# Kernel tuning notes

Hardware: AMD Instinct MI355X
Metric: run time of the kernel (lower is better)

Reference implementation:

```python
import jax, jax.numpy as jnp
import numpy as np

N_USER = 100000
N_ITEM = 50000
N_EDGE = 400000
D_IN = 128
N_HEADS = 4
D_HEAD = 32


def setup_inputs() -> dict:
    key = jax.random.key(0)
    ks = jax.random.split(key, 10)
    s = 1.0 / np.sqrt(D_IN)
    return {
        "h_user": jax.random.normal(ks[0], (N_USER, D_IN), jnp.float32),
        "h_item": jax.random.normal(ks[1], (N_ITEM, D_IN), jnp.float32),
        "edge_user": jax.random.randint(ks[2], (N_EDGE,), 0, N_USER),
        "edge_item": jax.random.randint(ks[3], (N_EDGE,), 0, N_ITEM),
        "user_w_qs": jax.random.normal(ks[4], (N_HEADS, D_IN, D_HEAD), jnp.float32) * s,
        "user_w_ks": jax.random.normal(ks[5], (N_HEADS, D_IN, D_HEAD), jnp.float32) * s,
        "user_w_vs": jax.random.normal(ks[6], (N_HEADS, D_IN, D_HEAD), jnp.float32) * s,
        "item_w_qs": jax.random.normal(ks[7], (N_HEADS, D_IN, D_HEAD), jnp.float32) * s,
        "item_w_ks": jax.random.normal(ks[8], (N_HEADS, D_IN, D_HEAD), jnp.float32) * s,
        "item_w_vs": jax.random.normal(ks[9], (N_HEADS, D_IN, D_HEAD), jnp.float32) * s,
    }


def _segment_softmax(logit, seg, num_segments):
    m = jax.ops.segment_max(logit, seg, num_segments=num_segments)
    e = jnp.exp(logit - m[seg])
    s = jax.ops.segment_sum(e, seg, num_segments=num_segments)
    return e / s[seg]


def _attend(src_idx, dst_idx, h_src, h_dst, w_qs, w_ks, w_vs, n_dst):
    # per-head projections: [H, n, d_head]
    q = jnp.einsum("nd,hde->hne", h_dst, w_qs)
    k = jnp.einsum("nd,hde->hne", h_src, w_ks)
    v = jnp.einsum("nd,hde->hne", h_src, w_vs)
    # per-edge logits: [H, E]
    logit = jnp.sum(q[:, dst_idx] * k[:, src_idx], axis=-1)
    att = jax.vmap(lambda l: _segment_softmax(l, dst_idx, n_dst))(logit)
    # sparse adj @ v == segment-sum of attention-weighted source values
    msg = att[..., None] * v[:, src_idx]  # [H, E, d_head]
    z = jax.vmap(lambda m: jax.ops.segment_sum(m, dst_idx, num_segments=n_dst))(msg)
    z = jax.nn.relu(z)  # nonlinear per head, then merge (concat)
    return jnp.transpose(z, (1, 0, 2)).reshape(n_dst, -1)


def reference(h_user, h_item, edge_user, edge_item,
              user_w_qs, user_w_ks, user_w_vs,
              item_w_qs, item_w_ks, item_w_vs):
    # i2u: items -> users (dst = users)
    z_user = _attend(edge_item, edge_user, h_item, h_user,
                     user_w_qs, item_w_ks, item_w_vs, N_USER)
    # u2i: users -> items (dst = items)
    z_item = _attend(edge_user, edge_item, h_user, h_item,
                     item_w_qs, user_w_ks, user_w_vs, N_ITEM)
    return (z_user, z_item)
```

## Files before the change

kernel.cpp:

```cpp
#include <hip/hip_runtime.h>
#include <hip/hip_fp16.h>


typedef unsigned short u16;
typedef float f32x4 __attribute__((ext_vector_type(4)));
typedef short bf16x8 __attribute__((ext_vector_type(8)));

#define NU_C    100000
#define NI_C    50000
#define E_C     400000
#define D_IN    128
#define D_HEAD  32
#define N_HEADS 4

#define PROJ_ROWS 64
#define PGU 1563
#define PGI 782
#define WT_BLKS 384

#define SCAN_T  256
#define SCAN_E  1024

__device__ __forceinline__ float bf2f(u16 b) {
    return __uint_as_float(((unsigned)b) << 16);
}

__device__ __forceinline__ u16 f2bf_rn(float x) {
    unsigned u = __float_as_uint(x);
    u += 0x7FFFu + ((u >> 16) & 1u);
    return (u16)(u >> 16);
}

__device__ __forceinline__ u16 f2h(float x) {
    return __half_as_ushort(__float2half(x));
}
__device__ __forceinline__ float h2f(u16 b) {
    return __half2float(__ushort_as_half(b));
}

__global__ void detect_dtypes(const void* __restrict__ h,
                              const void* __restrict__ eu,
                              int* __restrict__ flags) {
    int t = threadIdx.x;
    const u16* hw = (const u16*)h;
    int cnt = 0;
#pragma unroll
    for (int r = 0; r < 2; ++r) {
        int i = t + r * 64;
        unsigned ex = (hw[2 * i] >> 7) & 0xFFu;
        if (ex >= 118u && ex <= 137u) cnt++;
    }
    const int* ew = (const int*)eu;
    int nz = 0;
#pragma unroll
    for (int r = 0; r < 4; ++r) {
        int i = t + r * 64;
        if (ew[2 * i + 1] != 0) nz++;
    }
#pragma unroll
    for (int m = 1; m < 64; m <<= 1) {
        cnt += __shfl_xor(cnt, m);
        nz  += __shfl_xor(nz, m);
    }
    if (t == 0) {
        flags[0] = (cnt >= 64) ? 1 : 0;
        flags[1] = (nz == 0) ? 1 : 0;
        flags[2] = 0;
        flags[3] = 0;
    }
}

__global__ __launch_bounds__(256)
void prep(const void* __restrict__ w0, const void* __restrict__ w1,
          const void* __restrict__ w2, const void* __restrict__ w3,
          const void* __restrict__ w4, const void* __restrict__ w5,
          u16* __restrict__ wthi, u16* __restrict__ wtlo,
          const int* __restrict__ e_user, const int* __restrict__ e_item,
          int* __restrict__ du, int* __restrict__ di,
          int* __restrict__ degU, int* __restrict__ degI,
          int* __restrict__ flags) {
    int b = blockIdx.x;
    if (b < WT_BLKS) {
        int m = b >> 6;
        int f = (b & 63) * 256 + threadIdx.x;
        const void* ws[6] = { w0, w1, w2, w3, w4, w5 };
        const void* wp = ws[m];
        int head = f >> 12, e = f & 31;
        float x;
        if (flags[0]) x = bf2f(((const u16*)wp)[f]);
        else          x = ((const float*)wp)[f];
        u16 h = f2bf_rn(x);
        u16 l = f2bf_rn(x - bf2f(h));
        int o = m * 16384 + (head * 32 + e) * 128 + ((f >> 5) & 127);
        wthi[o] = h;
        wtlo[o] = l;
    } else {
        int g = (b - WT_BLKS) * 256 + threadIdx.x;
        if (g >= E_C) return;
        int is64 = flags[1];
        int u = is64 ? e_user[2 * g] : e_user[g];
        int i = is64 ? e_item[2 * g] : e_item[g];
        if ((unsigned)u >= (unsigned)NU_C) { atomicOr(&flags[3], 1); u = 0; }
        if ((unsigned)i >= (unsigned)NI_C) { atomicOr(&flags[3], 1); i = 0; }
        du[g] = u;
        di[g] = i;
        atomicAdd(&degU[u], 1);
        atomicAdd(&degI[i], 1);
    }
}

__global__ __launch_bounds__(SCAN_T)
void scan_pass1(const int* __restrict__ degU, int* __restrict__ offsU,
                int* __restrict__ partU, int nU, int sbU,
                const int* __restrict__ degI, int* __restrict__ offsI,
                int* __restrict__ partI, int nI) {
    __shared__ int tsum[SCAN_T];
    int t = threadIdx.x, b = blockIdx.x;
    const int* deg; int* offs; int* partials; int n; int lb;
    if (b < sbU) { deg = degU; offs = offsU; partials = partU; n = nU; lb = b; }
    else         { deg = degI; offs = offsI; partials = partI; n = nI; lb = b - sbU; }
    int idx = lb * SCAN_E + t * 4;
    int v0 = 0, v1 = 0, v2 = 0, v3 = 0;
    if (idx + 3 < n) {
        v0 = deg[idx]; v1 = deg[idx + 1]; v2 = deg[idx + 2]; v3 = deg[idx + 3];
    } else {
        if (idx     < n) v0 = deg[idx];
        if (idx + 1 < n) v1 = deg[idx + 1];
        if (idx + 2 < n) v2 = deg[idx + 2];
        if (idx + 3 < n) v3 = deg[idx + 3];
    }
    int s = v0 + v1 + v2 + v3;
    tsum[t] = s;
    __syncthreads();
#pragma unroll
    for (int o = 1; o < SCAN_T; o <<= 1) {
        int x = (t >= o) ? tsum[t - o] : 0;
        __syncthreads();
        tsum[t] += x;
        __syncthreads();
    }
    int run = tsum[t] - s;
    if (idx     < n) offs[idx]     = run;             run += v0;
    if (idx + 1 < n) offs[idx + 1] = run;             run += v1;
    if (idx + 2 < n) offs[idx + 2] = run;             run += v2;
    if (idx + 3 < n) offs[idx + 3] = run;
    if (t == SCAN_T - 1) partials[lb] = tsum[t];
}

__global__ __launch_bounds__(SCAN_T)
void scan_pass2(int* __restrict__ partU, int sbU,
                int* __restrict__ partI, int sbI) {
    __shared__ int tsum[SCAN_T];
    int t = threadIdx.x;
    int* partials; int nb;
    if (blockIdx.x == 0) { partials = partU; nb = sbU; }
    else                 { partials = partI; nb = sbI; }
    int v = (t < nb) ? partials[t] : 0;
    tsum[t] = v;
    __syncthreads();
#pragma unroll
    for (int o = 1; o < SCAN_T; o <<= 1) {
        int x = (t >= o) ? tsum[t - o] : 0;
        __syncthreads();
        tsum[t] += x;
        __syncthreads();
    }
    if (t < nb) partials[t] = tsum[t] - v;
}

__global__ void scatter2(const int* __restrict__ du, const int* __restrict__ di,
                         const int* __restrict__ offsU, const int* __restrict__ partU,
                         int* __restrict__ cntU, int* __restrict__ csrU,
                         const int* __restrict__ offsI, const int* __restrict__ partI,
                         int* __restrict__ cntI, int* __restrict__ csrI, int egrid) {
    int b = blockIdx.x;
    int g = (b >= egrid ? b - egrid : b) * 256 + threadIdx.x;
    if (g >= E_C) return;
    if (b < egrid) {
        int d = du[g];
        int pos = offsU[d] + partU[d >> 10] + atomicAdd(&cntU[d], 1);
        csrU[pos] = di[g];
    } else {
        int d = di[g];
        int pos = offsI[d] + partI[d >> 10] + atomicAdd(&cntI[d], 1);
        csrI[pos] = du[g];
    }
}

__global__ __launch_bounds__(256)
void proj6(const void* __restrict__ hu, const void* __restrict__ hi_,
           const u16* __restrict__ wthi_, const u16* __restrict__ wtlo_,
           u16* __restrict__ QU, u16* __restrict__ KI, u16* __restrict__ VI,
           u16* __restrict__ QI, u16* __restrict__ KU, u16* __restrict__ VU,
           const int* __restrict__ flags) {
    __shared__ u16 Hhi[PROJ_ROWS * 32], Hlo[PROJ_ROWS * 32];
    __shared__ u16 Bhi[128 * 32],       Blo[128 * 32];

    const int b = blockIdx.x;
    const void* hraw; const u16* wth; const u16* wtl; u16* out; int N; int lb;
    if (b < PGU) {
        hraw = hu;  wth = wthi_ + 0 * 16384; wtl = wtlo_ + 0 * 16384;
        out = QU; N = NU_C; lb = b;
    } else if (b < PGU + PGI) {
        hraw = hi_; wth = wthi_ + 4 * 16384; wtl = wtlo_ + 4 * 16384;
        out = KI; N = NI_C; lb = b - PGU;
    } else if (b < PGU + 2 * PGI) {
        hraw = hi_; wth = wthi_ + 5 * 16384; wtl = wtlo_ + 5 * 16384;
        out = VI; N = NI_C; lb = b - PGU - PGI;
    } else if (b < PGU + 3 * PGI) {
        hraw = hi_; wth = wthi_ + 3 * 16384; wtl = wtlo_ + 3 * 16384;
        out = QI; N = NI_C; lb = b - PGU - 2 * PGI;
    } else if (b < 2 * PGU + 3 * PGI) {
        hraw = hu;  wth = wthi_ + 1 * 16384; wtl = wtlo_ + 1 * 16384;
        out = KU; N = NU_C; lb = b - PGU - 3 * PGI;
    } else {
        hraw = hu;  wth = wthi_ + 2 * 16384; wtl = wtlo_ + 2 * 16384;
        out = VU; N = NU_C; lb = b - 2 * PGU - 3 * PGI;
    }

    const int t = threadIdx.x;
    const int n0 = lb * PROJ_ROWS;
    const int isbf = flags[0];

    const int srow = t >> 2, sq = t & 3;
    const int sgn = min(n0 + srow, N - 1);
    const int hbase = srow * 32 + ((sq ^ ((srow >> 1) & 3)) << 3);
    const int wj = t >> 1, wh = t & 1;
    const int wb0 = wj * 32 + (((wh * 2)     ^ ((wj >> 1) & 3)) << 3);
    const int wb1 = wj * 32 + (((wh * 2 + 1) ^ ((wj >> 1) & 3)) << 3);
    const int w = t >> 6, l = t & 63;
    const int lr = l & 15, lk = l >> 4;
    const int sc = (lk ^ ((lr >> 1) & 3)) << 3;

    f32x4 acc[4][2];
#pragma unroll
    for (int rt = 0; rt < 4; ++rt)
#pragma unroll
        for (int ci = 0; ci < 2; ++ci) {
            acc[rt][ci].x = 0.f; acc[rt][ci].y = 0.f;
            acc[rt][ci].z = 0.f; acc[rt][ci].w = 0.f;
        }

#define COMPUTE_STEP                                                           \
    do {                                                                       \
        bf16x8 fAh[4], fAl[4], fBh[2], fBl[2];                                 \
        _Pragma("unroll")                                                      \
        for (int rt = 0; rt < 4; ++rt) {                                       \
            int ar = (rt * 16 + lr) * 32 + sc;                                 \
            fAh[rt] = *(const bf16x8*)&Hhi[ar];                                \
            fAl[rt] = *(const bf16x8*)&Hlo[ar];                                \
        }                                                                      \
        _Pragma("unroll")                                                      \
        for (int ci = 0; ci < 2; ++ci) {                                       \
            int jr = ((w * 2 + ci) * 16 + lr) * 32 + sc;                       \
            fBh[ci] = *(const bf16x8*)&Bhi[jr];                                \
            fBl[ci] = *(const bf16x8*)&Blo[jr];                                \
        }                                                                      \
        _Pragma("unroll")                                                      \
        for (int rt = 0; rt < 4; ++rt)                                         \
        _Pragma("unroll")                                                      \
        for (int ci = 0; ci < 2; ++ci) {                                       \
            acc[rt][ci] = __builtin_amdgcn_mfma_f32_16x16x32_bf16(             \
                fAl[rt], fBh[ci], acc[rt][ci], 0, 0, 0);                       \
            acc[rt][ci] = __builtin_amdgcn_mfma_f32_16x16x32_bf16(             \
                fAh[rt], fBl[ci], acc[rt][ci], 0, 0, 0);                       \
            acc[rt][ci] = __builtin_amdgcn_mfma_f32_16x16x32_bf16(             \
                fAh[rt], fBh[ci], acc[rt][ci], 0, 0, 0);                       \
        }                                                                      \
    } while (0)

    if (!isbf) {
        const float* hp = (const float*)hraw;
        f32x4 rh0, rh1; bf16x8 rwh0, rwh1, rwl0, rwl1;
#define PLOAD(KC)                                                              \
        do {                                                                   \
            const float* hq = hp + (size_t)sgn * D_IN + (KC) * 32 + sq * 8;    \
            rh0 = *(const f32x4*)hq;                                           \
            rh1 = *(const f32x4*)(hq + 4);                                     \
            const u16* wp = wth + wj * 128 + (KC) * 32 + wh * 16;              \
            rwh0 = *(const bf16x8*)wp;  rwh1 = *(const bf16x8*)(wp + 8);       \
            const u16* lp = wtl + wj * 128 + (KC) * 32 + wh * 16;              \
            rwl0 = *(const bf16x8*)lp;  rwl1 = *(const bf16x8*)(lp + 8);       \
        } while (0)
        PLOAD(0);
        for (int kc = 0; kc < 4; ++kc) {
            if (kc) __syncthreads();
            bf16x8 hi8, lo8;
#pragma unroll
            for (int i = 0; i < 4; ++i) {
                u16 hh = f2bf_rn(rh0[i]);
                hi8[i] = (short)hh;
                lo8[i] = (short)f2bf_rn(rh0[i] - bf2f(hh));
            }
#pragma unroll
            for (int i = 0; i < 4; ++i) {
                u16 hh = f2bf_rn(rh1[i]);
                hi8[4 + i] = (short)hh;
                lo8[4 + i] = (short)f2bf_rn(rh1[i] - bf2f(hh));
            }
            *(bf16x8*)&Hhi[hbase] = hi8;
            *(bf16x8*)&Hlo[hbase] = lo8;
            *(bf16x8*)&Bhi[wb0] = rwh0;
            *(bf16x8*)&Bhi[wb1] = rwh1;
            *(bf16x8*)&Blo[wb0] = rwl0;
            *(bf16x8*)&Blo[wb1] = rwl1;
            __syncthreads();
            if (kc < 3) PLOAD(kc + 1);
            COMPUTE_STEP;
        }
#undef PLOAD
    } else {
        for (int kc = 0; kc < 4; ++kc) {
            if (kc) __syncthreads();
            bf16x8 hv = *(const bf16x8*)((const u16*)hraw
                        + (size_t)sgn * D_IN + kc * 32 + sq * 8);
            bf16x8 z;
#pragma unroll
            for (int i = 0; i < 8; ++i) z[i] = 0;
            *(bf16x8*)&Hhi[hbase] = hv;
            *(bf16x8*)&Hlo[hbase] = z;
            const u16* wp = wth + wj * 128 + kc * 32 + wh * 16;
            const u16* lp = wtl + wj * 128 + kc * 32 + wh * 16;
            *(bf16x8*)&Bhi[wb0] = *(const bf16x8*)wp;
            *(bf16x8*)&Bhi[wb1] = *(const bf16x8*)(wp + 8);
            *(bf16x8*)&Blo[wb0] = *(const bf16x8*)lp;
            *(bf16x8*)&Blo[wb1] = *(const bf16x8*)(lp + 8);
            __syncthreads();
            COMPUTE_STEP;
        }
    }
#undef COMPUTE_STEP

#pragma unroll
    for (int rt = 0; rt < 4; ++rt) {
#pragma unroll
        for (int r = 0; r < 4; ++r) {
            int n = n0 + rt * 16 + lk * 4 + r;
            if (n < N) {
#pragma unroll
                for (int ci = 0; ci < 2; ++ci)
                    out[(size_t)n * 128 + w * 32 + ci * 16 + lr] =
                        f2h(acc[rt][ci][r]);
            }
        }
    }
}

__global__ __launch_bounds__(256)
void gather_both(const int* __restrict__ offsU, const int* __restrict__ partU,
                 const int* __restrict__ csrU,
                 const int* __restrict__ offsI, const int* __restrict__ partI,
                 const int* __restrict__ csrI,
                 const u16* __restrict__ QU, const u16* __restrict__ KI,
                 const u16* __restrict__ VI,
                 const u16* __restrict__ QI, const u16* __restrict__ KU,
                 const u16* __restrict__ VU,
                 float* __restrict__ outbase, const int* __restrict__ flags,
                 int ggU) {
    int b = blockIdx.x;
    const int *offs, *part, *csr; const u16 *q, *k, *v;
    float* out; int Ndst; int g;
    if (b < ggU) {
        offs = offsU; part = partU; csr = csrU;
        q = QU; k = KI; v = VI; out = outbase; Ndst = NU_C;
        g = b * 256 + threadIdx.x;
    } else {
        offs = offsI; part = partI; csr = csrI;
        q = QI; k = KU; v = VU;
        out = outbase + (size_t)NU_C * 128; Ndst = NI_C;
        g = (b - ggU) * 256 + threadIdx.x;
    }
    int dst = g >> 6;
    if (dst >= Ndst) return;
    int l  = g & 63;
    int eh = l >> 5;
    int sl = l & 31;
    float* op = out + (size_t)dst * 128 + sl * 4;

    if (flags[3]) {
        if (eh == 0) {
            f32x4 d64; d64.x = d64.y = d64.z = d64.w = 64.0f;
            *(f32x4*)op = d64;
        }
        return;
    }

    ushort4 qu = *(const ushort4*)(q + (size_t)dst * 128 + sl * 4);
    f32x4 qv;
    qv.x = h2f(qu.x); qv.y = h2f(qu.y); qv.z = h2f(qu.z); qv.w = h2f(qu.w);
    f32x4 acc; acc.x = acc.y = acc.z = acc.w = 0.f;
    float ssum = 0.f;

    int e0 = offs[dst] + part[dst >> 10];
    int e1 = (dst + 1 == Ndst) ? E_C
             : offs[dst + 1] + part[(dst + 1) >> 10];
    int e = e0 + eh;
    for (; e + 2 < e1; e += 4) {
        int s0 = csr[e];
        int s1 = csr[e + 2];
        ushort4 ku0 = *(const ushort4*)(k + (size_t)s0 * 128 + sl * 4);
        ushort4 ku1 = *(const ushort4*)(k + (size_t)s1 * 128 + sl * 4);
        ushort4 vu0 = *(const ushort4*)(v + (size_t)s0 * 128 + sl * 4);
        ushort4 vu1 = *(const ushort4*)(v + (size_t)s1 * 128 + sl * 4);
        float d0 = qv.x * h2f(ku0.x) + qv.y * h2f(ku0.y)
                 + qv.z * h2f(ku0.z) + qv.w * h2f(ku0.w);
        float d1 = qv.x * h2f(ku1.x) + qv.y * h2f(ku1.y)
                 + qv.z * h2f(ku1.z) + qv.w * h2f(ku1.w);
        d0 += __shfl_xor(d0, 1);  d1 += __shfl_xor(d1, 1);
        d0 += __shfl_xor(d0, 2);  d1 += __shfl_xor(d1, 2);
        d0 += __shfl_xor(d0, 4);  d1 += __shfl_xor(d1, 4);
        float ev0 = __expf(fminf(fmaxf(d0, -80.f), 80.f));
        float ev1 = __expf(fminf(fmaxf(d1, -80.f), 80.f));
        ssum += ev0 + ev1;
        acc.x += ev0 * h2f(vu0.x) + ev1 * h2f(vu1.x);
        acc.y += ev0 * h2f(vu0.y) + ev1 * h2f(vu1.y);
        acc.z += ev0 * h2f(vu0.z) + ev1 * h2f(vu1.z);
        acc.w += ev0 * h2f(vu0.w) + ev1 * h2f(vu1.w);
    }
    if (e < e1) {
        int s = csr[e];
        ushort4 ku = *(const ushort4*)(k + (size_t)s * 128 + sl * 4);
        ushort4 vu = *(const ushort4*)(v + (size_t)s * 128 + sl * 4);
        float d = qv.x * h2f(ku.x) + qv.y * h2f(ku.y)
                + qv.z * h2f(ku.z) + qv.w * h2f(ku.w);
        d += __shfl_xor(d, 1);
        d += __shfl_xor(d, 2);
        d += __shfl_xor(d, 4);
        float ev = __expf(fminf(fmaxf(d, -80.f), 80.f));
        ssum += ev;
        acc.x += ev * h2f(vu.x); acc.y += ev * h2f(vu.y);
        acc.z += ev * h2f(vu.z); acc.w += ev * h2f(vu.w);
    }
    ssum  += __shfl_xor(ssum, 32);
    acc.x += __shfl_xor(acc.x, 32);
    acc.y += __shfl_xor(acc.y, 32);
    acc.z += __shfl_xor(acc.z, 32);
    acc.w += __shfl_xor(acc.w, 32);
    if (eh == 0) {
        float inv = (ssum > 0.f) ? (1.f / ssum) : 0.f;
        f32x4 o;
        o.x = fmaxf(acc.x * inv, 0.f);
        o.y = fmaxf(acc.y * inv, 0.f);
        o.z = fmaxf(acc.z * inv, 0.f);
        o.w = fmaxf(acc.w * inv, 0.f);
        *(f32x4*)op = o;
    }
}

__global__ void fill_diag(float* __restrict__ out, int n) {
    int g = blockIdx.x * 256 + threadIdx.x;
    if (g < n) out[g] = 48.0f;
}

extern "C" void kernel_launch(void* const* d_in, const int* in_sizes, int n_in,
                              void* d_out, int out_size, void* d_ws, size_t ws_size,
                              hipStream_t stream) {
    const void* h_user    = d_in[0];
    const void* h_item    = d_in[1];
    const int*  edge_user = (const int*)d_in[2];
    const int*  edge_item = (const int*)d_in[3];
    const void* u_wq = d_in[4];
    const void* u_wk = d_in[5];
    const void* u_wv = d_in[6];
    const void* i_wq = d_in[7];
    const void* i_wk = d_in[8];
    const void* i_wv = d_in[9];

    const int NU = NU_C, NI = NI_C;

    size_t szBufU = (((size_t)NU * 128 * 2) + 255) & ~(size_t)255;
    size_t szBufI = (((size_t)NI * 128 * 2) + 255) & ~(size_t)255;
    size_t szE    = (((size_t)E_C * 4) + 255) & ~(size_t)255;
    size_t szOffU = (((size_t)(NU + 1) * 4) + 255) & ~(size_t)255;
    size_t szOffI = (((size_t)(NI + 1) * 4) + 255) & ~(size_t)255;
    size_t szNU   = (((size_t)NU * 4) + 255) & ~(size_t)255;
    size_t szNI   = (((size_t)NI * 4) + 255) & ~(size_t)255;
    size_t szPart = 256 * 4;
    size_t szWt   = (size_t)6 * 16384 * 2;

    size_t off = 0;
    char* base = (char*)d_ws;
    u16* QU      = (u16*)(base + off);   off += szBufU;
    u16* KI      = (u16*)(base + off);   off += szBufI;
    u16* VI      = (u16*)(base + off);   off += szBufI;
    u16* QI      = (u16*)(base + off);   off += szBufI;
    u16* KU      = (u16*)(base + off);   off += szBufU;
    u16* VU      = (u16*)(base + off);   off += szBufU;
    int* du      = (int*)(base + off);   off += szE;
    int* di      = (int*)(base + off);   off += szE;
    int* csrU    = (int*)(base + off);   off += szE;
    int* csrI    = (int*)(base + off);   off += szE;
    int* offsU   = (int*)(base + off);   off += szOffU;
    int* offsI   = (int*)(base + off);   off += szOffI;
    int* partU   = (int*)(base + off);   off += szPart;
    int* partI   = (int*)(base + off);   off += szPart;
    u16* wthi    = (u16*)(base + off);   off += szWt;
    u16* wtlo    = (u16*)(base + off);   off += szWt;
    int* flags   = (int*)(base + off);   off += 256;
    size_t zoff = off;
    int* degU    = (int*)(base + off);   off += szNU;
    int* cntU    = (int*)(base + off);   off += szNU;
    int* degI    = (int*)(base + off);   off += szNI;
    int* cntI    = (int*)(base + off);   off += szNI;
    size_t need = off;

    if (need > ws_size) {
        fill_diag<<<(out_size + 255) / 256, 256, 0, stream>>>((float*)d_out, out_size);
        return;
    }

    int egrid = (E_C + 255) / 256;
    int sbU = (NU + SCAN_E - 1) / SCAN_E;
    int sbI = (NI + SCAN_E - 1) / SCAN_E;
    int ggU = (NU * 64 + 255) / 256;
    int ggI = (NI * 64 + 255) / 256;

    hipMemsetAsync(base + zoff, 0, need - zoff, stream);
    detect_dtypes<<<1, 64, 0, stream>>>(h_user, edge_user, flags);
    prep<<<WT_BLKS + egrid, 256, 0, stream>>>(
        u_wq, u_wk, u_wv, i_wq, i_wk, i_wv, wthi, wtlo,
        edge_user, edge_item, du, di, degU, degI, flags);
    scan_pass1<<<sbU + sbI, SCAN_T, 0, stream>>>(degU, offsU, partU, NU, sbU,
                                                 degI, offsI, partI, NI);
    scan_pass2<<<2, SCAN_T, 0, stream>>>(partU, sbU, partI, sbI);
    scatter2<<<2 * egrid, 256, 0, stream>>>(du, di,
                                            offsU, partU, cntU, csrU,
                                            offsI, partI, cntI, csrI, egrid);
    proj6<<<3 * PGU + 3 * PGI, 256, 0, stream>>>(
        h_user, h_item, wthi, wtlo, QU, KI, VI, QI, KU, VU, flags);
    gather_both<<<ggU + ggI, 256, 0, stream>>>(
        offsU, partU, csrU, offsI, partI, csrI,
        QU, KI, VI, QI, KU, VU, (float*)d_out, flags, ggU);
}
```

Measured before the change: 366.8 us.

## Replace LDS-tiled block projection with per-wave register-direct MFMA projection

The projection kernel is restructured so that each wavefront independently computes a 32-row by 128-column output tile. It loads activation and weight fragments straight from global memory into registers, with no shared-memory staging and no block barriers. This removes LDS traffic and __syncthreads between k-chunks. In exchange, weight tiles are re-read from global memory or cache by every wave, input rows are reused across fewer output columns per load, and register pressure rises from the 16 accumulators per lane.

```diff
diff --git a/kernel.cpp b/kernel.cpp
--- a/kernel.cpp
+++ b/kernel.cpp
@@ -13,9 +13,10 @@
 #define D_HEAD  32
 #define N_HEADS 4
 
-#define PROJ_ROWS 64
-#define PGU 1563
-#define PGI 782
+#define RBU 3125
+#define RBI 1563
+#define WU  (3 * RBU)
+#define WI  (3 * RBI)
 #define WT_BLKS 384
 
 #define SCAN_T  256
@@ -188,159 +189,103 @@
 }
 
 __global__ __launch_bounds__(256)
-void proj6(const void* __restrict__ hu, const void* __restrict__ hi_,
+void projw(const void* __restrict__ hu, const void* __restrict__ hi_,
            const u16* __restrict__ wthi_, const u16* __restrict__ wtlo_,
-           u16* __restrict__ QU, u16* __restrict__ KI, u16* __restrict__ VI,
-           u16* __restrict__ QI, u16* __restrict__ KU, u16* __restrict__ VU,
+           u16* __restrict__ QU, u16* __restrict__ KU, u16* __restrict__ VU,
+           u16* __restrict__ QI, u16* __restrict__ KI, u16* __restrict__ VI,
            const int* __restrict__ flags) {
-    __shared__ u16 Hhi[PROJ_ROWS * 32], Hlo[PROJ_ROWS * 32];
-    __shared__ u16 Bhi[128 * 32],       Blo[128 * 32];
-
-    const int b = blockIdx.x;
-    const void* hraw; const u16* wth; const u16* wtl; u16* out; int N; int lb;
-    if (b < PGU) {
-        hraw = hu;  wth = wthi_ + 0 * 16384; wtl = wtlo_ + 0 * 16384;
-        out = QU; N = NU_C; lb = b;
-    } else if (b < PGU + PGI) {
-        hraw = hi_; wth = wthi_ + 4 * 16384; wtl = wtlo_ + 4 * 16384;
-        out = KI; N = NI_C; lb = b - PGU;
-    } else if (b < PGU + 2 * PGI) {
-        hraw = hi_; wth = wthi_ + 5 * 16384; wtl = wtlo_ + 5 * 16384;
-        out = VI; N = NI_C; lb = b - PGU - PGI;
-    } else if (b < PGU + 3 * PGI) {
-        hraw = hi_; wth = wthi_ + 3 * 16384; wtl = wtlo_ + 3 * 16384;
-        out = QI; N = NI_C; lb = b - PGU - 2 * PGI;
-    } else if (b < 2 * PGU + 3 * PGI) {
-        hraw = hu;  wth = wthi_ + 1 * 16384; wtl = wtlo_ + 1 * 16384;
-        out = KU; N = NU_C; lb = b - PGU - 3 * PGI;
+    int wid = blockIdx.x * 4 + (threadIdx.x >> 6);
+    int l = threadIdx.x & 63;
+    const int lr = l & 15, lk = l >> 4;
+
+    const void* hraw; const u16* wth; const u16* wtl; u16* out; int N; int rb;
+    if (wid < WU) {
+        int m = wid / RBU; rb = wid - m * RBU;
+        hraw = hu; N = NU_C;
+        wth = wthi_ + m * 16384; wtl = wtlo_ + m * 16384;
+        out = (m == 0) ? QU : ((m == 1) ? KU : VU);
     } else {
-        hraw = hu;  wth = wthi_ + 2 * 16384; wtl = wtlo_ + 2 * 16384;
-        out = VU; N = NU_C; lb = b - 2 * PGU - 3 * PGI;
-    }
-
-    const int t = threadIdx.x;
-    const int n0 = lb * PROJ_ROWS;
+        int w2 = wid - WU;
+        int m = w2 / RBI; rb = w2 - m * RBI;
+        hraw = hi_; N = NI_C;
+        wth = wthi_ + (3 + m) * 16384; wtl = wtlo_ + (3 + m) * 16384;
+        out = (m == 0) ? QI : ((m == 1) ? KI : VI);
+    }
+
+    const int n0 = rb * 32;
+    const int row0 = min(n0 + lr, N - 1);
+    const int row1 = min(n0 + 16 + lr, N - 1);
     const int isbf = flags[0];
 
-    const int srow = t >> 2, sq = t & 3;
-    const int sgn = min(n0 + srow, N - 1);
-    const int hbase = srow * 32 + ((sq ^ ((srow >> 1) & 3)) << 3);
-    const int wj = t >> 1, wh = t & 1;
-    const int wb0 = wj * 32 + (((wh * 2)     ^ ((wj >> 1) & 3)) << 3);
-    const int wb1 = wj * 32 + (((wh * 2 + 1) ^ ((wj >> 1) & 3)) << 3);
-    const int w = t >> 6, l = t & 63;
-    const int lr = l & 15, lk = l >> 4;
-    const int sc = (lk ^ ((lr >> 1) & 3)) << 3;
-
-    f32x4 acc[4][2];
-#pragma unroll
-    for (int rt = 0; rt < 4; ++rt)
-#pragma unroll
-        for (int ci = 0; ci < 2; ++ci) {
-            acc[rt][ci].x = 0.f; acc[rt][ci].y = 0.f;
-            acc[rt][ci].z = 0.f; acc[rt][ci].w = 0.f;
+    f32x4 acc[2][8];
+#pragma unroll
+    for (int rt = 0; rt < 2; ++rt)
+#pragma unroll
+        for (int ct = 0; ct < 8; ++ct) {
+            acc[rt][ct].x = 0.f; acc[rt][ct].y = 0.f;
+            acc[rt][ct].z = 0.f; acc[rt][ct].w = 0.f;
         }
 
-#define COMPUTE_STEP                                                           \
-    do {                                                                       \
-        bf16x8 fAh[4], fAl[4], fBh[2], fBl[2];                                 \
-        _Pragma("unroll")                                                      \
-        for (int rt = 0; rt < 4; ++rt) {                                       \
-            int ar = (rt * 16 + lr) * 32 + sc;                                 \
-            fAh[rt] = *(const bf16x8*)&Hhi[ar];                                \
-            fAl[rt] = *(const bf16x8*)&Hlo[ar];                                \
-        }                                                                      \
-        _Pragma("unroll")                                                      \
-        for (int ci = 0; ci < 2; ++ci) {                                       \
-            int jr = ((w * 2 + ci) * 16 + lr) * 32 + sc;                       \
-            fBh[ci] = *(const bf16x8*)&Bhi[jr];                                \
-            fBl[ci] = *(const bf16x8*)&Blo[jr];                                \
-        }                                                                      \
-        _Pragma("unroll")                                                      \
-        for (int rt = 0; rt < 4; ++rt)                                         \
-        _Pragma("unroll")                                                      \
-        for (int ci = 0; ci < 2; ++ci) {                                       \
-            acc[rt][ci] = __builtin_amdgcn_mfma_f32_16x16x32_bf16(             \
-                fAl[rt], fBh[ci], acc[rt][ci], 0, 0, 0);                       \
-            acc[rt][ci] = __builtin_amdgcn_mfma_f32_16x16x32_bf16(             \
-                fAh[rt], fBl[ci], acc[rt][ci], 0, 0, 0);                       \
-            acc[rt][ci] = __builtin_amdgcn_mfma_f32_16x16x32_bf16(             \
-                fAh[rt], fBh[ci], acc[rt][ci], 0, 0, 0);                       \
-        }                                                                      \
-    } while (0)
-
-    if (!isbf) {
-        const float* hp = (const float*)hraw;
-        f32x4 rh0, rh1; bf16x8 rwh0, rwh1, rwl0, rwl1;
-#define PLOAD(KC)                                                              \
-        do {                                                                   \
-            const float* hq = hp + (size_t)sgn * D_IN + (KC) * 32 + sq * 8;    \
-            rh0 = *(const f32x4*)hq;                                           \
-            rh1 = *(const f32x4*)(hq + 4);                                     \
-            const u16* wp = wth + wj * 128 + (KC) * 32 + wh * 16;              \
-            rwh0 = *(const bf16x8*)wp;  rwh1 = *(const bf16x8*)(wp + 8);       \
-            const u16* lp = wtl + wj * 128 + (KC) * 32 + wh * 16;              \
-            rwl0 = *(const bf16x8*)lp;  rwl1 = *(const bf16x8*)(lp + 8);       \
-        } while (0)
-        PLOAD(0);
-        for (int kc = 0; kc < 4; ++kc) {
-            if (kc) __syncthreads();
-            bf16x8 hi8, lo8;
-#pragma unroll
-            for (int i = 0; i < 4; ++i) {
-                u16 hh = f2bf_rn(rh0[i]);
-                hi8[i] = (short)hh;
-                lo8[i] = (short)f2bf_rn(rh0[i] - bf2f(hh));
+#pragma unroll
+    for (int kc = 0; kc < 4; ++kc) {
+        const int kof = kc * 32 + lk * 8;
+        bf16x8 fAh[2], fAl[2];
+        if (!isbf) {
+            const float* hp = (const float*)hraw;
+#pragma unroll
+            for (int rt = 0; rt < 2; ++rt) {
+                const float* a = hp + (size_t)(rt ? row1 : row0) * D_IN + kof;
+                f32x4 a0 = *(const f32x4*)a;
+                f32x4 a1 = *(const f32x4*)(a + 4);
+#pragma unroll
+                for (int i = 0; i < 4; ++i) {
+                    u16 hh = f2bf_rn(a0[i]);
+                    fAh[rt][i] = (short)hh;
+                    fAl[rt][i] = (short)f2bf_rn(a0[i] - bf2f(hh));
+                }
+#pragma unroll
+                for (int i = 0; i < 4; ++i) {
+                    u16 hh = f2bf_rn(a1[i]);
+                    fAh[rt][4 + i] = (short)hh;
+                    fAl[rt][4 + i] = (short)f2bf_rn(a1[i] - bf2f(hh));
+                }
             }
-#pragma unroll
-            for (int i = 0; i < 4; ++i) {
-                u16 hh = f2bf_rn(rh1[i]);
-                hi8[4 + i] = (short)hh;
-                lo8[4 + i] = (short)f2bf_rn(rh1[i] - bf2f(hh));
+        } else {
+#pragma unroll
+            for (int rt = 0; rt < 2; ++rt) {
+                const u16* a = (const u16*)hraw
+                             + (size_t)(rt ? row1 : row0) * D_IN + kof;
+                fAh[rt] = *(const bf16x8*)a;
+#pragma unroll
+                for (int i = 0; i < 8; ++i) fAl[rt][i] = 0;
             }
-            *(bf16x8*)&Hhi[hbase] = hi8;
-            *(bf16x8*)&Hlo[hbase] = lo8;
-            *(bf16x8*)&Bhi[wb0] = rwh0;
-            *(bf16x8*)&Bhi[wb1] = rwh1;
-            *(bf16x8*)&Blo[wb0] = rwl0;
-            *(bf16x8*)&Blo[wb1] = rwl1;
-            __syncthreads();
-            if (kc < 3) PLOAD(kc + 1);
-            COMPUTE_STEP;
         }
-#undef PLOAD
-    } else {
-        for (int kc = 0; kc < 4; ++kc) {
-            if (kc) __syncthreads();
-            bf16x8 hv = *(const bf16x8*)((const u16*)hraw
-                        + (size_t)sgn * D_IN + kc * 32 + sq * 8);
-            bf16x8 z;
-#pragma unroll
-            for (int i = 0; i < 8; ++i) z[i] = 0;
-            *(bf16x8*)&Hhi[hbase] = hv;
-            *(bf16x8*)&Hlo[hbase] = z;
-            const u16* wp = wth + wj * 128 + kc * 32 + wh * 16;
-            const u16* lp = wtl + wj * 128 + kc * 32 + wh * 16;
-            *(bf16x8*)&Bhi[wb0] = *(const bf16x8*)wp;
-            *(bf16x8*)&Bhi[wb1] = *(const bf16x8*)(wp + 8);
-            *(bf16x8*)&Blo[wb0] = *(const bf16x8*)lp;
-            *(bf16x8*)&Blo[wb1] = *(const bf16x8*)(lp + 8);
-            __syncthreads();
-            COMPUTE_STEP;
+#pragma unroll
+        for (int ct = 0; ct < 8; ++ct) {
+            const size_t bo = (size_t)(ct * 16 + lr) * D_IN + kof;
+            bf16x8 fBh = *(const bf16x8*)(wth + bo);
+            bf16x8 fBl = *(const bf16x8*)(wtl + bo);
+#pragma unroll
+            for (int rt = 0; rt < 2; ++rt) {
+                acc[rt][ct] = __builtin_amdgcn_mfma_f32_16x16x32_bf16(
+                    fAl[rt], fBh, acc[rt][ct], 0, 0, 0);
+                acc[rt][ct] = __builtin_amdgcn_mfma_f32_16x16x32_bf16(
+                    fAh[rt], fBl, acc[rt][ct], 0, 0, 0);
+                acc[rt][ct] = __builtin_amdgcn_mfma_f32_16x16x32_bf16(
+                    fAh[rt], fBh, acc[rt][ct], 0, 0, 0);
+            }
         }
     }
-#undef COMPUTE_STEP
-
-#pragma unroll
-    for (int rt = 0; rt < 4; ++rt) {
+
+#pragma unroll
+    for (int rt = 0; rt < 2; ++rt) {
 #pragma unroll
         for (int r = 0; r < 4; ++r) {
             int n = n0 + rt * 16 + lk * 4 + r;
             if (n < N) {
 #pragma unroll
-                for (int ci = 0; ci < 2; ++ci)
-                    out[(size_t)n * 128 + w * 32 + ci * 16 + lr] =
-                        f2h(acc[rt][ci][r]);
+                for (int ct = 0; ct < 8; ++ct)
+                    out[(size_t)n * 128 + ct * 16 + lr] = f2h(acc[rt][ct][r]);
             }
         }
     }
@@ -514,6 +459,7 @@
     int sbI = (NI + SCAN_E - 1) / SCAN_E;
     int ggU = (NU * 64 + 255) / 256;
     int ggI = (NI * 64 + 255) / 256;
+    int pwb = (WU + WI + 3) / 4;
 
     hipMemsetAsync(base + zoff, 0, need - zoff, stream);
     detect_dtypes<<<1, 64, 0, stream>>>(h_user, edge_user, flags);
@@ -526,8 +472,8 @@
     scatter2<<<2 * egrid, 256, 0, stream>>>(du, di,
                                             offsU, partU, cntU, csrU,
                                             offsI, partI, cntI, csrI, egrid);
-    proj6<<<3 * PGU + 3 * PGI, 256, 0, stream>>>(
-        h_user, h_item, wthi, wtlo, QU, KI, VI, QI, KU, VU, flags);
+    projw<<<pwb, 256, 0, stream>>>(
+        h_user, h_item, wthi, wtlo, QU, KU, VU, QI, KI, VI, flags);
     gather_both<<<ggU + ggI, 256, 0, stream>>>(
         offsU, partU, csrU, offsI, partI, csrI,
         QU, KI, VI, QI, KU, VU, (float*)d_out, flags, ggU);
```

Result: slower. 430.8 us (+17.5%).
